# Kernel optimization log

Hardware: AMD Instinct MI355X
Metric: run time of the kernel (lower is better)

## Reference

```python
import jax, jax.numpy as jnp
import numpy as np

K, D, B = 512, 64, 4096  # n_primitives, view_dim, batch
TRIL_I, TRIL_J = np.tril_indices(D, -1)  # matches torch.tril_indices(D, D, offset=-1)
EPS = 1e-8


def setup_inputs() -> dict:
    key = jax.random.key(0)
    k1, k2, k3 = jax.random.split(key, 3)
    z = jax.random.normal(k1, (B, D), dtype=jnp.float32)
    # _init_weights: mu ~ N(0, 1/sqrt(D)) (random_normal mode)
    mu = jax.random.normal(k2, (K, D), dtype=jnp.float32) / np.float32(np.sqrt(D))
    # log_diag = 2*log(precision_init_scale) = 0 for scale=1, no jitter
    log_diag = jnp.zeros((K, D), dtype=jnp.float32)
    # point_softmax mode -> log_s zero-init
    log_s = jnp.zeros((K,), dtype=jnp.float32)
    # full covariance: lower_offdiag ~ N(0, offdiag_init_std=0.01)
    lower_offdiag = 0.01 * jax.random.normal(k3, (K, D * (D - 1) // 2), dtype=jnp.float32)
    return {"z": z, "mu": mu, "log_diag": log_diag, "log_s": log_s,
            "lower_offdiag": lower_offdiag}


def _precision_cholesky(log_diag, lower_offdiag):
    # (K, D, D) lower-triangular Cholesky factor of the precision matrix
    chol = jnp.zeros((K, D, D), dtype=log_diag.dtype)
    didx = jnp.arange(D)
    chol = chol.at[:, didx, didx].set(jnp.exp(0.5 * log_diag))
    chol = chol.at[:, TRIL_I, TRIL_J].set(lower_offdiag)
    return chol


def reference(z, mu, log_diag, log_s, lower_offdiag):
    chol = _precision_cholesky(log_diag, lower_offdiag)          # (K, D, D)
    diff = z[:, None, :] - mu[None, :, :]                        # (B, K, D)
    transformed = jnp.einsum('bkd,kde->bke', diff, chol)         # (B, K, D)
    mahal = jnp.sum(transformed * transformed, axis=-1)          # (B, K)
    strength = jax.nn.softplus(log_s)                            # (K,)
    log_a = -0.5 * mahal + jnp.log(strength + EPS)[None, :]
    log_a_max = jax.lax.stop_gradient(jnp.max(log_a, axis=-1, keepdims=True))
    a = jnp.exp(log_a - log_a_max)
    alpha = a / (jnp.sum(a, axis=-1, keepdims=True) + EPS)       # (B, K)
    return alpha
```

## Files before the change

kernel.cpp:

```cpp
#include <hip/hip_runtime.h>
#include <hip/hip_bf16.h>
#include <math.h>

#define KP   512
#define DD   64
#define BB   4096
#define NTRI 2016

typedef __attribute__((ext_vector_type(8))) short bfrag;
typedef __attribute__((ext_vector_type(4))) float facc4;


__device__ __forceinline__ void async16(const void* g, void* l) {
    __builtin_amdgcn_global_load_lds(
        (const __attribute__((address_space(1))) unsigned int*)g,
        (__attribute__((address_space(3))) unsigned int*)l, 16, 0, 0);
}

__global__ __launch_bounds__(256) void prep_kernel(
    const float* __restrict__ mu, const float* __restrict__ log_diag,
    const float* __restrict__ log_s, const float* __restrict__ lod,
    unsigned short* __restrict__ Limg, float* __restrict__ wws,
    float* __restrict__ biasws)
{
    const int k = blockIdx.x;
    const int tid = threadIdx.x;
    __shared__ float Lc[64 * 64];
    __shared__ float muS[64];
    __shared__ float wp[4][64];

    for (int idx = tid; idx < 4096; idx += 256) Lc[idx] = 0.0f;
    if (tid < 64) muS[tid] = mu[k * 64 + tid];
    __syncthreads();

    if (tid < 64) Lc[tid * 64 + tid] = expf(0.5f * log_diag[k * 64 + tid]);
    for (int t = tid; t < NTRI; t += 256) {
        int i = (int)((1.0f + sqrtf(8.0f * (float)t + 1.0f)) * 0.5f);
        while (i * (i - 1) / 2 > t) --i;
        while ((i + 1) * i / 2 <= t) ++i;
        int j = t - i * (i - 1) / 2;
        Lc[j * 64 + i] = lod[(size_t)k * NTRI + t];
    }
    __syncthreads();

    {
        const int e = tid & 63, part = tid >> 6;
        float s = 0.0f;
        for (int d = e + part; d < 64; d += 4)
            s += muS[d] * Lc[e * 64 + d];
        wp[part][e] = s;
    }
    __syncthreads();
    if (tid < 64)
        wws[k * 64 + tid] = -(wp[0][tid] + wp[1][tid] + wp[2][tid] + wp[3][tid]);

    for (int idx = tid; idx < 4096; idx += 256) {
        int e = idx >> 6, d = idx & 63;
        int sw = (e << 6) | (d ^ ((e & 7) << 3));
        __hip_bfloat16 hb = __float2bfloat16(Lc[idx]);
        Limg[(size_t)k * 4096 + sw] = *(unsigned short*)&hb;
    }
    if (tid == 0) {
        float s = log_s[k];
        float sp = (s > 20.0f) ? s : log1pf(expf(s));
        biasws[k] = logf(sp + 1e-8f);
    }
}

__global__ __launch_bounds__(256) void mahal_kernel(
    const float* __restrict__ z, const unsigned short* __restrict__ Limg,
    const float* __restrict__ wws, float* __restrict__ mahal)
{
    __shared__ __align__(16) char  ldsImg[3][8192];
    __shared__ __align__(16) float wS[16 * 64];

    const int tid  = threadIdx.x;
    const int wave = tid >> 6;
    const int lane = tid & 63;
    const int g    = lane >> 4;
    const int l15  = lane & 15;

    const int n      = blockIdx.x;
    const int kslice = (n & 7) + ((n >> 8) << 3);
    const int bblk   = (n >> 3) & 31;
    const int k0     = kslice * 16;
    const int bw     = bblk * 128 + wave * 32;

    const char* imgK = (const char*)Limg + (size_t)k0 * 8192;

#pragma unroll
    for (int b0 = 0; b0 < 2; ++b0) {
        const char* src = imgK + (size_t)b0 * 8192;
        char* dst = &ldsImg[b0][0];
#pragma unroll
        for (int p = 0; p < 2; ++p) {
            const int cof = p * 4096 + wave * 1024;
            async16(src + cof + lane * 16, dst + cof);
        }
    }

    for (int i = tid; i < 16 * 64; i += 256) wS[i] = wws[k0 * 64 + i];

    bfrag zh[2][2], zl[2][2];
#pragma unroll
    for (int bs = 0; bs < 2; ++bs) {
        const float* zp = z + (size_t)(bw + bs * 16 + l15) * 64 + 8 * g;
#pragma unroll
        for (int ds = 0; ds < 2; ++ds) {
            float4 a = *(const float4*)(zp + ds * 32);
            float4 c = *(const float4*)(zp + ds * 32 + 4);
            float vv[8] = {a.x, a.y, a.z, a.w, c.x, c.y, c.z, c.w};
            bfrag th, tl;
#pragma unroll
            for (int j = 0; j < 8; ++j) {
                __hip_bfloat16 hb = __float2bfloat16(vv[j]);
                float hv = __bfloat162float(hb);
                __hip_bfloat16 lb = __float2bfloat16(vv[j] - hv);
                th[j] = *(short*)&hb;
                tl[j] = *(short*)&lb;
            }
            zh[bs][ds] = th;
            zl[bs][ds] = tl;
        }
    }

    const int swz = (l15 & 7) << 4;

    __syncthreads();

    for (int t = 0; t < 16; ++t) {
        __builtin_amdgcn_s_barrier();

        if (t + 2 < 16) {
            const char* src = imgK + (size_t)(t + 2) * 8192;
            char* dst = &ldsImg[(t + 2) % 3][0];
#pragma unroll
            for (int p = 0; p < 2; ++p) {
                const int cof = p * 4096 + wave * 1024;
                async16(src + cof + lane * 16, dst + cof);
            }
        }

        if (t < 14)       asm volatile("s_waitcnt vmcnt(8)" ::: "memory");
        else if (t == 14) asm volatile("s_waitcnt vmcnt(6)" ::: "memory");
        else              asm volatile("s_waitcnt vmcnt(4)" ::: "memory");
        __builtin_amdgcn_s_barrier();

        const char* buf = &ldsImg[t % 3][0];

        const float* wrow = wS + t * 64;
        facc4 wv[4];
#pragma unroll
        for (int et = 0; et < 4; ++et)
            wv[et] = *(const facc4*)(wrow + et * 16 + 4 * g);

        facc4 acc[4][2];

        __builtin_amdgcn_s_setprio(1);
#pragma unroll
        for (int ds = 0; ds < 2; ++ds) {
#pragma unroll
            for (int et = 0; et < 4; ++et) {
                if (et >= 2 && ds == 0) continue;
                const bool first = (ds == 0) ? (et < 2) : (et >= 2);
                const int ao = et * 2048 + l15 * 128 + ((ds * 64 + 16 * g) ^ swz);
                bfrag lh = *(const bfrag*)(buf + ao);
#pragma unroll
                for (int bs = 0; bs < 2; ++bs) {
                    acc[et][bs] = __builtin_amdgcn_mfma_f32_16x16x32_bf16(
                        lh, zh[bs][ds], first ? wv[et] : acc[et][bs], 0, 0, 0);
                    acc[et][bs] = __builtin_amdgcn_mfma_f32_16x16x32_bf16(
                        lh, zl[bs][ds], acc[et][bs], 0, 0, 0);
                }
            }
        }
        __builtin_amdgcn_s_setprio(0);

        const int k = k0 + t;
#pragma unroll
        for (int bs = 0; bs < 2; ++bs) {
            float p0 = 0.f, p1 = 0.f, p2 = 0.f, p3 = 0.f;
#pragma unroll
            for (int et = 0; et < 4; ++et) {
                p0 = fmaf(acc[et][bs][0], acc[et][bs][0], p0);
                p1 = fmaf(acc[et][bs][1], acc[et][bs][1], p1);
                p2 = fmaf(acc[et][bs][2], acc[et][bs][2], p2);
                p3 = fmaf(acc[et][bs][3], acc[et][bs][3], p3);
            }
            float s = (p0 + p1) + (p2 + p3);
            s += __shfl_xor(s, 16, 64);
            s += __shfl_xor(s, 32, 64);
            if (g == 0)
                mahal[(size_t)(bw + bs * 16 + l15) * KP + k] = s;
        }
    }
}

__global__ __launch_bounds__(256) void softmax_kernel(
    const float* __restrict__ mahal, const float* __restrict__ biasws,
    float* __restrict__ alpha)
{
    const int tid  = threadIdx.x;
    const int lane = tid & 63;
    const int b    = blockIdx.x * 4 + (tid >> 6);

    const float* mrow = mahal + (size_t)b * KP + lane * 8;
    const float* brow = biasws + lane * 8;
    float4 m0 = *(const float4*)(mrow);
    float4 m1 = *(const float4*)(mrow + 4);
    float4 c0 = *(const float4*)(brow);
    float4 c1 = *(const float4*)(brow + 4);

    float la[8];
    la[0] = fmaf(-0.5f, m0.x, c0.x); la[1] = fmaf(-0.5f, m0.y, c0.y);
    la[2] = fmaf(-0.5f, m0.z, c0.z); la[3] = fmaf(-0.5f, m0.w, c0.w);
    la[4] = fmaf(-0.5f, m1.x, c1.x); la[5] = fmaf(-0.5f, m1.y, c1.y);
    la[6] = fmaf(-0.5f, m1.z, c1.z); la[7] = fmaf(-0.5f, m1.w, c1.w);

    float lm = la[0];
#pragma unroll
    for (int j = 1; j < 8; ++j) lm = fmaxf(lm, la[j]);
#pragma unroll
    for (int off = 32; off >= 1; off >>= 1)
        lm = fmaxf(lm, __shfl_xor(lm, off, 64));

    float a[8], s = 0.0f;
#pragma unroll
    for (int j = 0; j < 8; ++j) { a[j] = expf(la[j] - lm); s += a[j]; }
#pragma unroll
    for (int off = 32; off >= 1; off >>= 1)
        s += __shfl_xor(s, off, 64);

    const float r = 1.0f / (s + 1e-8f);
    float4 o0 = {a[0] * r, a[1] * r, a[2] * r, a[3] * r};
    float4 o1 = {a[4] * r, a[5] * r, a[6] * r, a[7] * r};
    float* orow = alpha + (size_t)b * KP + lane * 8;
    *(float4*)(orow)     = o0;
    *(float4*)(orow + 4) = o1;
}

extern "C" void kernel_launch(void* const* d_in, const int* in_sizes, int n_in,
                              void* d_out, int out_size, void* d_ws, size_t ws_size,
                              hipStream_t stream) {
    const float* z        = (const float*)d_in[0];
    const float* mu       = (const float*)d_in[1];
    const float* log_diag = (const float*)d_in[2];
    const float* log_s    = (const float*)d_in[3];
    const float* lod      = (const float*)d_in[4];
    float* out = (float*)d_out;

    char* ws = (char*)d_ws;
    unsigned short* Limg = (unsigned short*)ws;
    float* wws    = (float*)(ws + (size_t)KP * 8192);
    float* biasws = wws + (size_t)KP * 64;
    float* mahalws = biasws + KP;

    prep_kernel<<<KP, 256, 0, stream>>>(mu, log_diag, log_s, lod, Limg, wws, biasws);
    mahal_kernel<<<1024, 256, 0, stream>>>(z, Limg, wws, mahalws);
    softmax_kernel<<<BB / 4, 256, 0, stream>>>(mahalws, biasws, out);
}
```

Measured before the change: 46.90 us.

## Process two primitives per pipeline stage with double-buffered LDS and paired stores

The mahal kernel now loads the Cholesky images for two primitives (16 KB) per stage into a two-deep LDS double buffer, replacing the three-deep single-primitive ring. This halves the number of barrier/wait iterations. The two mahal results per row are also written as one float2 store instead of two scalar stores. LDS use grows from 24 KB to 32 KB per block, which may lower occupancy, and the prefetch distance shrinks to one stage ahead.

```diff
diff --git a/kernel.cpp b/kernel.cpp
--- a/kernel.cpp
+++ b/kernel.cpp
@@ -71,7 +71,7 @@
     const float* __restrict__ z, const unsigned short* __restrict__ Limg,
     const float* __restrict__ wws, float* __restrict__ mahal)
 {
-    __shared__ __align__(16) char  ldsImg[3][8192];
+    __shared__ __align__(16) char  ldsImg[2][16384];
     __shared__ __align__(16) float wS[16 * 64];
 
     const int tid  = threadIdx.x;
@@ -89,14 +89,9 @@
     const char* imgK = (const char*)Limg + (size_t)k0 * 8192;
 
 #pragma unroll
-    for (int b0 = 0; b0 < 2; ++b0) {
-        const char* src = imgK + (size_t)b0 * 8192;
-        char* dst = &ldsImg[b0][0];
-#pragma unroll
-        for (int p = 0; p < 2; ++p) {
-            const int cof = p * 4096 + wave * 1024;
-            async16(src + cof + lane * 16, dst + cof);
-        }
+    for (int p4 = 0; p4 < 4; ++p4) {
+        const int cof = p4 * 4096 + wave * 1024;
+        async16(imgK + cof + lane * 16, &ldsImg[0][0] + cof);
     }
 
     for (int i = tid; i < 16 * 64; i += 256) wS[i] = wws[k0 * 64 + i];
@@ -128,70 +123,79 @@
 
     __syncthreads();
 
-    for (int t = 0; t < 16; ++t) {
+    for (int p = 0; p < 8; ++p) {
         __builtin_amdgcn_s_barrier();
 
-        if (t + 2 < 16) {
-            const char* src = imgK + (size_t)(t + 2) * 8192;
-            char* dst = &ldsImg[(t + 2) % 3][0];
-#pragma unroll
-            for (int p = 0; p < 2; ++p) {
-                const int cof = p * 4096 + wave * 1024;
+        if (p < 7) {
+            const char* src = imgK + (size_t)(p + 1) * 16384;
+            char* dst = &ldsImg[(p + 1) & 1][0];
+#pragma unroll
+            for (int p4 = 0; p4 < 4; ++p4) {
+                const int cof = p4 * 4096 + wave * 1024;
                 async16(src + cof + lane * 16, dst + cof);
             }
         }
 
-        if (t < 14)       asm volatile("s_waitcnt vmcnt(8)" ::: "memory");
-        else if (t == 14) asm volatile("s_waitcnt vmcnt(6)" ::: "memory");
-        else              asm volatile("s_waitcnt vmcnt(4)" ::: "memory");
+        if (p == 0)      asm volatile("s_waitcnt vmcnt(4)" ::: "memory");
+        else if (p < 7)  asm volatile("s_waitcnt vmcnt(6)" ::: "memory");
+        else             asm volatile("s_waitcnt vmcnt(2)" ::: "memory");
         __builtin_amdgcn_s_barrier();
 
-        const char* buf = &ldsImg[t % 3][0];
-
-        const float* wrow = wS + t * 64;
-        facc4 wv[4];
-#pragma unroll
-        for (int et = 0; et < 4; ++et)
-            wv[et] = *(const facc4*)(wrow + et * 16 + 4 * g);
-
-        facc4 acc[4][2];
-
-        __builtin_amdgcn_s_setprio(1);
-#pragma unroll
-        for (int ds = 0; ds < 2; ++ds) {
-#pragma unroll
-            for (int et = 0; et < 4; ++et) {
-                if (et >= 2 && ds == 0) continue;
-                const bool first = (ds == 0) ? (et < 2) : (et >= 2);
-                const int ao = et * 2048 + l15 * 128 + ((ds * 64 + 16 * g) ^ swz);
-                bfrag lh = *(const bfrag*)(buf + ao);
-#pragma unroll
-                for (int bs = 0; bs < 2; ++bs) {
-                    acc[et][bs] = __builtin_amdgcn_mfma_f32_16x16x32_bf16(
-                        lh, zh[bs][ds], first ? wv[et] : acc[et][bs], 0, 0, 0);
-                    acc[et][bs] = __builtin_amdgcn_mfma_f32_16x16x32_bf16(
-                        lh, zl[bs][ds], acc[et][bs], 0, 0, 0);
+        const char* buf = &ldsImg[p & 1][0];
+        float2 sres[2];
+
+#pragma unroll
+        for (int k2 = 0; k2 < 2; ++k2) {
+            const float* wrow = wS + (p * 2 + k2) * 64;
+            facc4 wv[4];
+#pragma unroll
+            for (int et = 0; et < 4; ++et)
+                wv[et] = *(const facc4*)(wrow + et * 16 + 4 * g);
+
+            facc4 acc[4][2];
+
+            __builtin_amdgcn_s_setprio(1);
+#pragma unroll
+            for (int ds = 0; ds < 2; ++ds) {
+#pragma unroll
+                for (int et = 0; et < 4; ++et) {
+                    if (et >= 2 && ds == 0) continue;
+                    const bool first = (ds == 0) ? (et < 2) : (et >= 2);
+                    const int ao = k2 * 8192 + et * 2048 + l15 * 128
+                                 + ((ds * 64 + 16 * g) ^ swz);
+                    bfrag lh = *(const bfrag*)(buf + ao);
+#pragma unroll
+                    for (int bs = 0; bs < 2; ++bs) {
+                        acc[et][bs] = __builtin_amdgcn_mfma_f32_16x16x32_bf16(
+                            lh, zh[bs][ds], first ? wv[et] : acc[et][bs], 0, 0, 0);
+                        acc[et][bs] = __builtin_amdgcn_mfma_f32_16x16x32_bf16(
+                            lh, zl[bs][ds], acc[et][bs], 0, 0, 0);
+                    }
                 }
             }
-        }
-        __builtin_amdgcn_s_setprio(0);
-
-        const int k = k0 + t;
+            __builtin_amdgcn_s_setprio(0);
+
+#pragma unroll
+            for (int bs = 0; bs < 2; ++bs) {
+                float p0 = 0.f, p1 = 0.f, p2 = 0.f, p3 = 0.f;
+#pragma unroll
+                for (int et = 0; et < 4; ++et) {
+                    p0 = fmaf(acc[et][bs][0], acc[et][bs][0], p0);
+                    p1 = fmaf(acc[et][bs][1], acc[et][bs][1], p1);
+                    p2 = fmaf(acc[et][bs][2], acc[et][bs][2], p2);
+                    p3 = fmaf(acc[et][bs][3], acc[et][bs][3], p3);
+                }
+                float s = (p0 + p1) + (p2 + p3);
+                s += __shfl_xor(s, 16, 64);
+                s += __shfl_xor(s, 32, 64);
+                if (k2 == 0) sres[bs].x = s; else sres[bs].y = s;
+            }
+        }
+
 #pragma unroll
         for (int bs = 0; bs < 2; ++bs) {
-            float p0 = 0.f, p1 = 0.f, p2 = 0.f, p3 = 0.f;
-#pragma unroll
-            for (int et = 0; et < 4; ++et) {
-                p0 = fmaf(acc[et][bs][0], acc[et][bs][0], p0);
-                p1 = fmaf(acc[et][bs][1], acc[et][bs][1], p1);
-                p2 = fmaf(acc[et][bs][2], acc[et][bs][2], p2);
-                p3 = fmaf(acc[et][bs][3], acc[et][bs][3], p3);
-            }
-            float s = (p0 + p1) + (p2 + p3);
-            s += __shfl_xor(s, 16, 64);
-            s += __shfl_xor(s, 32, 64);
             if (g == 0)
-                mahal[(size_t)(bw + bs * 16 + l15) * KP + k] = s;
+                *(float2*)(mahal + (size_t)(bw + bs * 16 + l15) * KP + k0 + 2 * p) = sres[bs];
         }
     }
 }
```

New measurement: 51.07 us. 8.9% more time.
